# Performance work log

Hardware: AMD Instinct MI355X
Metric: run time of the kernel (lower is better)

## Reference

```python
import jax, jax.numpy as jnp
import numpy as np

N = 100000
E = 600000
IN_DIM = 128
OUT_DIM = 256
BN_EPS = 1e-5


def setup_inputs() -> dict:
    key = jax.random.key(0)
    ks = jax.random.split(key, 12)
    x = jax.random.normal(ks[0], (N, IN_DIM), dtype=jnp.float32)
    edge_index = jax.random.randint(ks[1], (2, E), 0, N, dtype=jnp.int64)
    s1 = 1.0 / np.sqrt(IN_DIM)
    s2 = 1.0 / np.sqrt(OUT_DIM)
    return {
        "x": x,
        "edge_index": edge_index,
        "eps": jnp.zeros((), dtype=jnp.float32),  # GINConv eps init = 0
        "W1": jax.random.uniform(ks[2], (IN_DIM, OUT_DIM), jnp.float32, -s1, s1),
        "b1": jnp.zeros((OUT_DIM,), jnp.float32),
        "W2": jax.random.uniform(ks[3], (OUT_DIM, OUT_DIM), jnp.float32, -s2, s2),
        "b2": jnp.zeros((OUT_DIM,), jnp.float32),
        "gamma": jnp.ones((OUT_DIM,), jnp.float32),
        "beta": jnp.zeros((OUT_DIM,), jnp.float32),
        "run_mean": jnp.zeros((OUT_DIM,), jnp.float32),
        "run_var": jnp.ones((OUT_DIM,), jnp.float32),
        "Wp": jax.random.uniform(ks[4], (IN_DIM, OUT_DIM), jnp.float32, -s1, s1),
        "bp": jnp.zeros((OUT_DIM,), jnp.float32),
    }


def reference(x, edge_index, eps, W1, b1, W2, b2, gamma, beta, run_mean, run_var, Wp, bp):
    src, dst = edge_index[0], edge_index[1]
    # GIN aggregation: sum_{j in N(i)} x_j  (scatter-add of source features to dst)
    agg = jax.ops.segment_sum(x[src], dst, num_segments=N)
    h = (1.0 + eps) * x + agg            # [N, in_dim]
    # 2-layer MLP (nn1)
    h = jax.nn.relu(h @ W1 + b1) @ W2 + b2   # [N, out_dim]
    # BatchNorm1d (eval mode: running stats); dropout = identity (eval)
    h = (h - run_mean) * jax.lax.rsqrt(run_var + BN_EPS) * gamma + beta
    # residual with projection (in_dim != out_dim)
    return h + x @ Wp + bp
```

## Files before the change

### kernel.cpp

```cpp
#include <hip/hip_runtime.h>

#define N_ 100000
#define E_ 600000
#define IND_ 128
#define OUTD_ 256
#define NT_ (N_/16)
#define NB_ 98
#define CASTN_ (N_*IND_/2)

typedef __attribute__((ext_vector_type(8))) short bf16x8;
typedef __attribute__((ext_vector_type(4))) float f32x4;
typedef __attribute__((ext_vector_type(2))) unsigned int u32x2;

static __device__ __forceinline__ unsigned f2bf_u(float f){
  union { float f; unsigned u; } v; v.f = f;
  return (v.u + 0x7fffu + ((v.u >> 16) & 1u)) >> 16;
}
static __device__ __forceinline__ unsigned pack2(float a, float b){
  return f2bf_u(a) | (f2bf_u(b) << 16);
}
static __device__ __forceinline__ float blo(unsigned u){
  union { unsigned u; float f; } v; v.u = u << 16; return v.f;
}
static __device__ __forceinline__ float bhi(unsigned u){
  union { unsigned u; float f; } v; v.u = u & 0xffff0000u; return v.f;
}
static __device__ __forceinline__ void gload_lds16(const bf16x8* g, bf16x8* l){
  __builtin_amdgcn_global_load_lds((const __attribute__((address_space(1))) void*)g,
                                   (__attribute__((address_space(3))) void*)l, 16, 0, 0);
}

__global__ void k_prep(const float* __restrict__ x,
                       const float* __restrict__ W1, const float* __restrict__ W2,
                       const float* __restrict__ Wp, const float* __restrict__ b2,
                       const float* __restrict__ gamma, const float* __restrict__ beta,
                       const float* __restrict__ mean, const float* __restrict__ var,
                       const float* __restrict__ bp,
                       const int* __restrict__ dst, int* __restrict__ deg,
                       unsigned short* __restrict__ W1s, unsigned short* __restrict__ W2s,
                       unsigned short* __restrict__ Wps,
                       float* __restrict__ scale, float* __restrict__ shift,
                       unsigned* __restrict__ xbw)
{
  int gid = blockIdx.x*256 + threadIdx.x;
  if (gid < 16384) {
    const float* W; unsigned short* Ws; int u;
    if (gid < 4096)       { W = W1; Ws = W1s; u = gid; }
    else if (gid < 12288) { W = W2; Ws = W2s; u = gid - 4096; }
    else                  { W = Wp; Ws = Wps; u = gid - 12288; }
    int l  = u & 63;
    int km = (u >> 6) & 1;
    int t  = (u >> 7) & 15;
    int q  = u >> 11;
    int kk = 2*q + km;
    int kb = kk*32 + (l >> 4)*8;
    int c  = 16*t + (l & 15);
    #pragma unroll
    for (int j = 0; j < 8; j++)
      Ws[u*8 + j] = (unsigned short)f2bf_u(W[(size_t)(kb + j)*OUTD_ + c]);
  } else if (gid < 16640) {
    int c = gid - 16384;
    float s = gamma[c] * rsqrtf(var[c] + 1e-5f);
    scale[c] = s;
    shift[c] = (b2[c] - mean[c]) * s + beta[c] + bp[c];
  } else if (gid < 16640 + CASTN_) {
    int ci = gid - 16640;
    float2 v = ((const float2*)x)[ci];
    xbw[ci] = pack2(v.x, v.y);
  } else if (gid < 16640 + CASTN_ + E_) {
    int e = gid - 16640 - CASTN_;
    atomicAdd(&deg[dst[e]], 1);
  }
}

__global__ __launch_bounds__(1024) void k_scan1(const int* __restrict__ deg,
                                                int* __restrict__ bsum, int* __restrict__ offs){
  __shared__ int red[16];
  int tid = threadIdx.x;
  int i = blockIdx.x*1024 + tid;
  int v = (i < N_) ? deg[i] : 0;
  #pragma unroll
  for (int d = 32; d; d >>= 1) v += __shfl_down(v, d);
  if ((tid & 63) == 0) red[tid >> 6] = v;
  __syncthreads();
  if (tid < 16) {
    int s = red[tid];
    #pragma unroll
    for (int d = 8; d; d >>= 1) s += __shfl_down(s, d, 16);
    if (tid == 0) bsum[blockIdx.x] = s;
  }
  if (blockIdx.x == 0 && tid == 0) offs[N_] = E_;
}

__global__ __launch_bounds__(1024) void k_scan2(const int* __restrict__ deg,
                                                const int* __restrict__ bsum, int* __restrict__ offs){
  __shared__ int bs[128];
  __shared__ int d1[1024];
  int tid = threadIdx.x;
  if (tid < 128) bs[tid] = (tid < NB_) ? bsum[tid] : 0;
  __syncthreads();
  #pragma unroll
  for (int d = 1; d < 128; d <<= 1){
    int v = (tid < 128 && tid >= d) ? bs[tid - d] : 0;
    __syncthreads();
    if (tid < 128) bs[tid] += v;
    __syncthreads();
  }
  int bprefix = (blockIdx.x > 0) ? bs[blockIdx.x - 1] : 0;
  int i = blockIdx.x*1024 + tid;
  int v = (i < N_) ? deg[i] : 0;
  d1[tid] = v;
  __syncthreads();
  #pragma unroll
  for (int d = 1; d < 1024; d <<= 1){
    int t = (tid >= d) ? d1[tid - d] : 0;
    __syncthreads();
    d1[tid] += t;
    __syncthreads();
  }
  if (i < N_) offs[i] = bprefix + d1[tid] - v;
}

__global__ void k_fill(const int* __restrict__ src, const int* __restrict__ dst,
                       const int* __restrict__ offs, int* __restrict__ cur, int* __restrict__ adj){
  int e = blockIdx.x*256 + threadIdx.x;
  if (e < E_) {
    int d = dst[e];
    int p = atomicAdd(&cur[d], 1);
    adj[offs[d] + p] = src[e];
  }
}

__global__ void k_agg(const unsigned* __restrict__ xb32, const int* __restrict__ offs,
                      const int* __restrict__ adj, const float* __restrict__ epsp,
                      unsigned* __restrict__ h0)
{
  int row  = blockIdx.x*4 + (threadIdx.x >> 6);
  int lane = threadIdx.x & 63;
  if (row >= N_) return;
  unsigned xw = xb32[(size_t)row*64 + lane];
  float ax0=0,ay0=0,ax1=0,ay1=0,ax2=0,ay2=0,ax3=0,ay3=0;
  float ax4=0,ay4=0,ax5=0,ay5=0,ax6=0,ay6=0,ax7=0,ay7=0;
  int b = offs[row], e = offs[row+1];
  for (int base = b; base < e; base += 64){
    int cnt = min(64, e - base);
    int idx = adj[base + min(lane, cnt - 1)];
    int j = 0;
    for (; j + 8 <= cnt; j += 8){
      int n0 = __shfl(idx, j+0), n1 = __shfl(idx, j+1);
      int n2 = __shfl(idx, j+2), n3 = __shfl(idx, j+3);
      int n4 = __shfl(idx, j+4), n5 = __shfl(idx, j+5);
      int n6 = __shfl(idx, j+6), n7 = __shfl(idx, j+7);
      unsigned v0 = xb32[(size_t)n0*64 + lane];
      unsigned v1 = xb32[(size_t)n1*64 + lane];
      unsigned v2 = xb32[(size_t)n2*64 + lane];
      unsigned v3 = xb32[(size_t)n3*64 + lane];
      unsigned v4 = xb32[(size_t)n4*64 + lane];
      unsigned v5 = xb32[(size_t)n5*64 + lane];
      unsigned v6 = xb32[(size_t)n6*64 + lane];
      unsigned v7 = xb32[(size_t)n7*64 + lane];
      ax0 += blo(v0); ay0 += bhi(v0);
      ax1 += blo(v1); ay1 += bhi(v1);
      ax2 += blo(v2); ay2 += bhi(v2);
      ax3 += blo(v3); ay3 += bhi(v3);
      ax4 += blo(v4); ay4 += bhi(v4);
      ax5 += blo(v5); ay5 += bhi(v5);
      ax6 += blo(v6); ay6 += bhi(v6);
      ax7 += blo(v7); ay7 += bhi(v7);
    }
    for (; j < cnt; j++){
      int n = __shfl(idx, j);
      unsigned v = xb32[(size_t)n*64 + lane];
      ax0 += blo(v); ay0 += bhi(v);
    }
  }
  float ax = ((ax0+ax1)+(ax2+ax3)) + ((ax4+ax5)+(ax6+ax7));
  float ay = ((ay0+ay1)+(ay2+ay3)) + ((ay4+ay5)+(ay6+ay7));
  float k1 = 1.f + epsp[0];
  h0[(size_t)row*64 + lane] = pack2(fmaf(k1, blo(xw), ax), fmaf(k1, bhi(xw), ay));
}

__global__ __launch_bounds__(256) void k_mlp(const unsigned short* __restrict__ h0,
        const unsigned short* __restrict__ xb16,
        const bf16x8* __restrict__ W1s, const float* __restrict__ b1,
        const bf16x8* __restrict__ W2s, const bf16x8* __restrict__ Wps,
        const float* __restrict__ scale, const float* __restrict__ shift,
        float* __restrict__ out)
{
  __shared__ bf16x8 w[2][2048];
  __shared__ __align__(16) char trans[4][2][1280];
  int tid = threadIdx.x;
  int wv = tid >> 6, lane = tid & 63, g = lane >> 4, r = lane & 15;
  int tile0 = blockIdx.x*4 + wv;
  int tile  = min(tile0, NT_ - 1);

  const bf16x8* hrow = (const bf16x8*)(h0 + ((size_t)tile*16 + r)*IND_);
  const bf16x8* xrow = (const bf16x8*)(xb16 + ((size_t)tile*16 + r)*IND_);
  bf16x8 B[4], XV[4];
  #pragma unroll
  for (int kk = 0; kk < 4; kk++) B[kk] = hrow[kk*4 + g];
  #pragma unroll
  for (int kk = 0; kk < 4; kk++) XV[kk] = xrow[kk*4 + g];

  auto STAGE = [&](int buf, const bf16x8* src){
    #pragma unroll
    for (int i = 0; i < 8; i++)
      gload_lds16(&src[i*256 + wv*64 + lane], &w[buf][i*256 + wv*64]);
  };
  f32x4 acc[16];
  auto MF = [&](int buf, bf16x8 f0, bf16x8 f1){
    #pragma unroll
    for (int t = 0; t < 16; t++)
      acc[t] = __builtin_amdgcn_mfma_f32_16x16x32_bf16(w[buf][(t*2+0)*64 + lane], f0, acc[t], 0,0,0);
    #pragma unroll
    for (int t = 0; t < 16; t++)
      acc[t] = __builtin_amdgcn_mfma_f32_16x16x32_bf16(w[buf][(t*2+1)*64 + lane], f1, acc[t], 0,0,0);
  };
  #pragma unroll
  for (int t = 0; t < 16; t++) acc[t] = (f32x4){0.f,0.f,0.f,0.f};

  STAGE(0, W1s);
  __syncthreads();

  STAGE(1, W1s + 2048);
  MF(0, B[0], B[1]);
  __syncthreads();

  STAGE(0, W2s);
  MF(1, B[2], B[3]);

  const float4* b1v = (const float4*)b1;
  bf16x8 H[8];
  #pragma unroll
  for (int kkh = 0; kkh < 8; kkh++){
    char* tr = &trans[wv][kkh & 1][0];
    #pragma unroll
    for (int h = 0; h < 2; h++){
      int t = 2*kkh + h;
      float4 bb = b1v[t*4 + g];
      f32x4 a = acc[t];
      float v0 = fmaxf(a.x + bb.x, 0.f);
      float v1 = fmaxf(a.y + bb.y, 0.f);
      float v2 = fmaxf(a.z + bb.z, 0.f);
      float v3 = fmaxf(a.w + bb.w, 0.f);
      u32x2 dd; dd.x = pack2(v0, v1); dd.y = pack2(v2, v3);
      *(u32x2*)(tr + r*80 + h*32 + g*8) = dd;
    }
    H[kkh] = *(const bf16x8*)(tr + r*80 + g*16);
  }
  #pragma unroll
  for (int t = 0; t < 16; t++) acc[t] = (f32x4){0.f,0.f,0.f,0.f};
  __syncthreads();

  STAGE(1, W2s + 2048);
  MF(0, H[0], H[1]);
  __syncthreads();

  STAGE(0, W2s + 4096);
  MF(1, H[2], H[3]);
  __syncthreads();

  STAGE(1, W2s + 6144);
  MF(0, H[4], H[5]);
  __syncthreads();

  STAGE(0, Wps);
  MF(1, H[6], H[7]);
  __syncthreads();

  STAGE(1, Wps + 2048);
  MF(0, XV[0], XV[1]);
  __syncthreads();

  MF(1, XV[2], XV[3]);

  if (tile0 < NT_){
    const float4* sc = (const float4*)scale;
    const float4* sh = (const float4*)shift;
    #pragma unroll
    for (int t = 0; t < 16; t++){
      float4 s = sc[t*4 + g], b = sh[t*4 + g];
      f32x4 a = acc[t];
      float4 o;
      o.x = fmaf(a.x, s.x, b.x);
      o.y = fmaf(a.y, s.y, b.y);
      o.z = fmaf(a.z, s.z, b.z);
      o.w = fmaf(a.w, s.w, b.w);
      *(float4*)(out + ((size_t)tile*16 + r)*OUTD_ + t*16 + g*4) = o;
    }
  }
}

extern "C" void kernel_launch(void* const* d_in, const int* in_sizes, int n_in,
                              void* d_out, int out_size, void* d_ws, size_t ws_size,
                              hipStream_t stream)
{
  const float* x     = (const float*)d_in[0];
  const int*   ei    = (const int*)d_in[1];
  const float* eps   = (const float*)d_in[2];
  const float* W1    = (const float*)d_in[3];
  const float* b1    = (const float*)d_in[4];
  const float* W2    = (const float*)d_in[5];
  const float* b2    = (const float*)d_in[6];
  const float* gamma = (const float*)d_in[7];
  const float* beta  = (const float*)d_in[8];
  const float* rmean = (const float*)d_in[9];
  const float* rvar  = (const float*)d_in[10];
  const float* Wp    = (const float*)d_in[11];
  const float* bp    = (const float*)d_in[12];
  float* out = (float*)d_out;

  char* ws = (char*)d_ws; size_t off = 0;
  auto carve = [&](size_t b)->char* { char* p = ws + off; off = (off + b + 255) & ~(size_t)255; return p; };
  unsigned*       xbuf  = (unsigned*)carve((size_t)CASTN_*4);
  unsigned*       h0    = (unsigned*)carve((size_t)N_*64*4);
  unsigned short* W1s   = (unsigned short*)carve(4096*16);
  unsigned short* W2s   = (unsigned short*)carve(8192*16);
  unsigned short* Wps   = (unsigned short*)carve(4096*16);
  float*          scale = (float*)carve(256*4);
  float*          shift = (float*)carve(256*4);
  int*            deg   = (int*)carve((size_t)N_*4);
  int*            cur   = (int*)carve((size_t)N_*4);
  int*            offs  = (int*)carve((size_t)(N_+1)*4);
  int*            adj   = (int*)carve((size_t)E_*4);
  int*            bsum  = (int*)carve((size_t)NB_*4);

  hipMemsetAsync(deg, 0, (size_t)N_*4, stream);
  hipMemsetAsync(cur, 0, (size_t)N_*4, stream);

  k_prep <<<(16640 + CASTN_ + E_ + 255)/256, 256, 0, stream>>>(x, W1, W2, Wp, b2, gamma, beta,
                                  rmean, rvar, bp, ei + E_, deg,
                                  W1s, W2s, Wps, scale, shift, xbuf);
  k_scan1<<<NB_, 1024, 0, stream>>>(deg, bsum, offs);
  k_scan2<<<NB_, 1024, 0, stream>>>(deg, bsum, offs);
  k_fill <<<(E_+255)/256, 256, 0, stream>>>(ei, ei + E_, offs, cur, adj);
  k_agg  <<<(N_+3)/4, 256, 0, stream>>>(xbuf, offs, adj, eps, h0);
  k_mlp  <<<(NT_+3)/4, 256, 0, stream>>>((const unsigned short*)h0, (const unsigned short*)xbuf,
                                         (const bf16x8*)W1s, b1, (const bf16x8*)W2s,
                                         (const bf16x8*)Wps, scale, shift, out);
}
```

Before: 196.0 us.

## Balance aggregation by splitting each block's edge range evenly across waves with LDS atomics

The aggregation kernel now assigns 32 rows per block and splits that block's CSR edge range evenly across its four waves, instead of one wave per row. Each edge carries its destination index (adjacency becomes int2 pairs), and partial sums go into shared-memory float atomics before a final write of the row results. The aim is to remove load imbalance from varying node degrees and idle lanes on short rows. The cost is larger adjacency traffic, LDS atomic overhead per edge, and extra shuffles.

```diff
diff --git a/kernel.cpp b/kernel.cpp
--- a/kernel.cpp
+++ b/kernel.cpp
@@ -7,6 +7,7 @@
 #define NT_ (N_/16)
 #define NB_ 98
 #define CASTN_ (N_*IND_/2)
+#define RPB_ 32
 
 typedef __attribute__((ext_vector_type(8))) short bf16x8;
 typedef __attribute__((ext_vector_type(4))) float f32x4;
@@ -122,62 +123,77 @@
 }
 
 __global__ void k_fill(const int* __restrict__ src, const int* __restrict__ dst,
-                       const int* __restrict__ offs, int* __restrict__ cur, int* __restrict__ adj){
+                       const int* __restrict__ offs, int* __restrict__ cur, int2* __restrict__ adjd){
   int e = blockIdx.x*256 + threadIdx.x;
   if (e < E_) {
     int d = dst[e];
     int p = atomicAdd(&cur[d], 1);
-    adj[offs[d] + p] = src[e];
-  }
-}
-
-__global__ void k_agg(const unsigned* __restrict__ xb32, const int* __restrict__ offs,
-                      const int* __restrict__ adj, const float* __restrict__ epsp,
-                      unsigned* __restrict__ h0)
+    adjd[offs[d] + p] = make_int2(src[e], d);
+  }
+}
+
+__global__ __launch_bounds__(256) void k_agg(const unsigned* __restrict__ xb32,
+                      const int* __restrict__ offs, const int2* __restrict__ adjd,
+                      const float* __restrict__ epsp, unsigned* __restrict__ h0)
 {
-  int row  = blockIdx.x*4 + (threadIdx.x >> 6);
-  int lane = threadIdx.x & 63;
-  if (row >= N_) return;
-  unsigned xw = xb32[(size_t)row*64 + lane];
-  float ax0=0,ay0=0,ax1=0,ay1=0,ax2=0,ay2=0,ax3=0,ay3=0;
-  float ax4=0,ay4=0,ax5=0,ay5=0,ax6=0,ay6=0,ax7=0,ay7=0;
-  int b = offs[row], e = offs[row+1];
-  for (int base = b; base < e; base += 64){
-    int cnt = min(64, e - base);
-    int idx = adj[base + min(lane, cnt - 1)];
+  __shared__ float hacc[RPB_][2][64];
+  int tid = threadIdx.x, wv = tid >> 6, lane = tid & 63;
+  int rb = blockIdx.x * RPB_;
+
+  float4* hz = (float4*)&hacc[0][0][0];
+  #pragma unroll
+  for (int i = 0; i < 4; i++) hz[tid + i*256] = (float4){0.f,0.f,0.f,0.f};
+  __syncthreads();
+
+  int eb = offs[rb], ee = offs[rb + RPB_];
+  int len = ee - eb;
+  int ws = eb + ((len * wv) >> 2);
+  int we = eb + ((len * (wv+1)) >> 2);
+
+  for (int base = ws; base < we; base += 64){
+    int cnt = min(64, we - base);
+    int2 ed = adjd[base + min(lane, cnt - 1)];
     int j = 0;
     for (; j + 8 <= cnt; j += 8){
-      int n0 = __shfl(idx, j+0), n1 = __shfl(idx, j+1);
-      int n2 = __shfl(idx, j+2), n3 = __shfl(idx, j+3);
-      int n4 = __shfl(idx, j+4), n5 = __shfl(idx, j+5);
-      int n6 = __shfl(idx, j+6), n7 = __shfl(idx, j+7);
-      unsigned v0 = xb32[(size_t)n0*64 + lane];
-      unsigned v1 = xb32[(size_t)n1*64 + lane];
-      unsigned v2 = xb32[(size_t)n2*64 + lane];
-      unsigned v3 = xb32[(size_t)n3*64 + lane];
-      unsigned v4 = xb32[(size_t)n4*64 + lane];
-      unsigned v5 = xb32[(size_t)n5*64 + lane];
-      unsigned v6 = xb32[(size_t)n6*64 + lane];
-      unsigned v7 = xb32[(size_t)n7*64 + lane];
-      ax0 += blo(v0); ay0 += bhi(v0);
-      ax1 += blo(v1); ay1 += bhi(v1);
-      ax2 += blo(v2); ay2 += bhi(v2);
-      ax3 += blo(v3); ay3 += bhi(v3);
-      ax4 += blo(v4); ay4 += bhi(v4);
-      ax5 += blo(v5); ay5 += bhi(v5);
-      ax6 += blo(v6); ay6 += bhi(v6);
-      ax7 += blo(v7); ay7 += bhi(v7);
+      int s0=__shfl(ed.x,j+0), s1=__shfl(ed.x,j+1), s2=__shfl(ed.x,j+2), s3=__shfl(ed.x,j+3);
+      int s4=__shfl(ed.x,j+4), s5=__shfl(ed.x,j+5), s6=__shfl(ed.x,j+6), s7=__shfl(ed.x,j+7);
+      int d0=__shfl(ed.y,j+0), d1=__shfl(ed.y,j+1), d2=__shfl(ed.y,j+2), d3=__shfl(ed.y,j+3);
+      int d4=__shfl(ed.y,j+4), d5=__shfl(ed.y,j+5), d6=__shfl(ed.y,j+6), d7=__shfl(ed.y,j+7);
+      unsigned v0 = xb32[(size_t)s0*64 + lane];
+      unsigned v1 = xb32[(size_t)s1*64 + lane];
+      unsigned v2 = xb32[(size_t)s2*64 + lane];
+      unsigned v3 = xb32[(size_t)s3*64 + lane];
+      unsigned v4 = xb32[(size_t)s4*64 + lane];
+      unsigned v5 = xb32[(size_t)s5*64 + lane];
+      unsigned v6 = xb32[(size_t)s6*64 + lane];
+      unsigned v7 = xb32[(size_t)s7*64 + lane];
+      atomicAdd(&hacc[d0-rb][0][lane], blo(v0)); atomicAdd(&hacc[d0-rb][1][lane], bhi(v0));
+      atomicAdd(&hacc[d1-rb][0][lane], blo(v1)); atomicAdd(&hacc[d1-rb][1][lane], bhi(v1));
+      atomicAdd(&hacc[d2-rb][0][lane], blo(v2)); atomicAdd(&hacc[d2-rb][1][lane], bhi(v2));
+      atomicAdd(&hacc[d3-rb][0][lane], blo(v3)); atomicAdd(&hacc[d3-rb][1][lane], bhi(v3));
+      atomicAdd(&hacc[d4-rb][0][lane], blo(v4)); atomicAdd(&hacc[d4-rb][1][lane], bhi(v4));
+      atomicAdd(&hacc[d5-rb][0][lane], blo(v5)); atomicAdd(&hacc[d5-rb][1][lane], bhi(v5));
+      atomicAdd(&hacc[d6-rb][0][lane], blo(v6)); atomicAdd(&hacc[d6-rb][1][lane], bhi(v6));
+      atomicAdd(&hacc[d7-rb][0][lane], blo(v7)); atomicAdd(&hacc[d7-rb][1][lane], bhi(v7));
     }
     for (; j < cnt; j++){
-      int n = __shfl(idx, j);
-      unsigned v = xb32[(size_t)n*64 + lane];
-      ax0 += blo(v); ay0 += bhi(v);
+      int s = __shfl(ed.x, j), d = __shfl(ed.y, j);
+      unsigned v = xb32[(size_t)s*64 + lane];
+      atomicAdd(&hacc[d-rb][0][lane], blo(v));
+      atomicAdd(&hacc[d-rb][1][lane], bhi(v));
     }
   }
-  float ax = ((ax0+ax1)+(ax2+ax3)) + ((ax4+ax5)+(ax6+ax7));
-  float ay = ((ay0+ay1)+(ay2+ay3)) + ((ay4+ay5)+(ay6+ay7));
+  __syncthreads();
+
   float k1 = 1.f + epsp[0];
-  h0[(size_t)row*64 + lane] = pack2(fmaf(k1, blo(xw), ax), fmaf(k1, bhi(xw), ay));
+  #pragma unroll
+  for (int k = 0; k < 8; k++){
+    int rl = wv*8 + k;
+    int row = rb + rl;
+    unsigned xw = xb32[(size_t)row*64 + lane];
+    h0[(size_t)row*64 + lane] = pack2(fmaf(k1, blo(xw), hacc[rl][0][lane]),
+                                      fmaf(k1, bhi(xw), hacc[rl][1][lane]));
+  }
 }
 
 __global__ __launch_bounds__(256) void k_mlp(const unsigned short* __restrict__ h0,
@@ -322,7 +338,7 @@
   int*            deg   = (int*)carve((size_t)N_*4);
   int*            cur   = (int*)carve((size_t)N_*4);
   int*            offs  = (int*)carve((size_t)(N_+1)*4);
-  int*            adj   = (int*)carve((size_t)E_*4);
+  int2*           adjd  = (int2*)carve((size_t)E_*8);
   int*            bsum  = (int*)carve((size_t)NB_*4);
 
   hipMemsetAsync(deg, 0, (size_t)N_*4, stream);
@@ -333,8 +349,8 @@
                                   W1s, W2s, Wps, scale, shift, xbuf);
   k_scan1<<<NB_, 1024, 0, stream>>>(deg, bsum, offs);
   k_scan2<<<NB_, 1024, 0, stream>>>(deg, bsum, offs);
-  k_fill <<<(E_+255)/256, 256, 0, stream>>>(ei, ei + E_, offs, cur, adj);
-  k_agg  <<<(N_+3)/4, 256, 0, stream>>>(xbuf, offs, adj, eps, h0);
+  k_fill <<<(E_+255)/256, 256, 0, stream>>>(ei, ei + E_, offs, cur, adjd);
+  k_agg  <<<N_/RPB_, 256, 0, stream>>>(xbuf, offs, adjd, eps, h0);
   k_mlp  <<<(NT_+3)/4, 256, 0, stream>>>((const unsigned short*)h0, (const unsigned short*)xbuf,
                                          (const bf16x8*)W1s, b1, (const bf16x8*)W2s,
                                          (const bf16x8*)Wps, scale, shift, out);
```

After: 583.2 us. 198% more time.
